# Kernel tuning notes

Measured on AMD Instinct MI355X. Metric: run time of the kernel, lower is better.

The kernel has to match this reference:

```python
import jax, jax.numpy as jnp
import numpy as np

BUCKET_SIZE = 256
LOOK_BACKWARD = 1
LOOK_FORWARD = 0  # causal


def look_around(x, backward, forward, pad_value):
    # x: (b, n_buckets, w, ...) -> (b, n_buckets, w*(backward+forward+1), ...)
    n = x.shape[1]
    pads = [(0, 0)] * x.ndim
    pads[1] = (backward, forward)
    p = jnp.pad(x, pads, constant_values=pad_value)
    return jnp.concatenate([p[:, i:i + n] for i in range(backward + forward + 1)], axis=2)


def setup_inputs() -> dict:
    key = jax.random.key(0)
    kq, kk, kv = jax.random.split(key, 3)
    shape = (2, 16, 4096, 64)  # [batch, heads, seq, head_dim]
    q = jax.random.normal(kq, shape, dtype=jnp.float32)
    k = jax.random.normal(kk, shape, dtype=jnp.float32)
    v = jax.random.normal(kv, shape, dtype=jnp.float32)
    return {"q": q, "k": k, "v": v}


def reference(q, k, v):
    shape = q.shape
    t, e = shape[-2], shape[-1]
    merge = lambda x: x.reshape(-1, t, e)
    q, k, v = merge(q), merge(k), merge(v)
    b = q.shape[0]
    buckets = t // BUCKET_SIZE

    bucket_fn = lambda x: x.reshape(b, buckets, BUCKET_SIZE, e)
    bq, bk, bv = bucket_fn(q), bucket_fn(k), bucket_fn(v)

    bk = look_around(bk, LOOK_BACKWARD, LOOK_FORWARD, 0.0)
    bv = look_around(bv, LOOK_BACKWARD, LOOK_FORWARD, 0.0)

    ticker = jnp.arange(t, dtype=jnp.int32).reshape(1, buckets, BUCKET_SIZE)
    bq_t = ticker  # (1, buckets, w)
    bq_k = look_around(ticker, LOOK_BACKWARD, LOOK_FORWARD, -1)  # (1, buckets, w*(lb+lf+1))

    dots = jnp.einsum('bnie,bnje->bnij', bq, bk) * (e ** -0.5)
    mask_value = -jnp.finfo(dots.dtype).max

    causal_mask = bq_t[:, :, :, None] < bq_k[:, :, None, :]
    pad_mask = (bq_k == -1)[:, :, None, :]
    dots = jnp.where(causal_mask | pad_mask, mask_value, dots)

    attn = jax.nn.softmax(dots, axis=-1)
    out = jnp.einsum('bnij,bnje->bnie', attn, bv)
    return out.reshape(shape)
```

## Files before the change

### kernel.cpp

```cpp
#include <hip/hip_runtime.h>

typedef __bf16 bf16x8 __attribute__((ext_vector_type(8)));
typedef float f32x4 __attribute__((ext_vector_type(4)));
typedef unsigned int u32;
typedef unsigned short u16;

#define KB 64
#define NCH 8
#define KSTR 72
#define PSP 72
#define VPS 68

static __device__ __forceinline__ u32 pack_bf2(float a, float b) {
    u16 x = __builtin_bit_cast(u16, (__bf16)a);
    u16 y = __builtin_bit_cast(u16, (__bf16)b);
    return (u32)x | ((u32)y << 16);
}

__global__ __launch_bounds__(512)
void local_attn_kernel(const float* __restrict__ qg, const float* __restrict__ kg,
                       const float* __restrict__ vg, float* __restrict__ og)
{
    __shared__ __align__(16) __bf16 sK[KB][KSTR];
    __shared__ __align__(16) u32    sVp[32][VPS];
    __shared__ __align__(16) __bf16 sP[8][2][16][PSP];

    const int bid = ((blockIdx.x & 7) << 6) | (blockIdx.x >> 3);
    const int bh = bid >> 4, bi = bid & 15;
    const int tid = threadIdx.x, w = tid >> 6;
    const int lane = tid & 63, lo = lane & 15, hi = lane >> 4;

    const long long base = (long long)bh << 18;
    const float* qb = qg + base + ((long long)bi << 14);
    const float* kb = kg + base + (((long long)(bi - 1)) << 14);
    const float* vb = vg + base + (((long long)(bi - 1)) << 14);
    float*       ob = og + base + ((long long)bi << 14);

    bf16x8 qa[2][2];
#pragma unroll
    for (int mt = 0; mt < 2; ++mt)
#pragma unroll
      for (int kk = 0; kk < 2; ++kk) {
        const float* src = qb + (w * 32 + mt * 16 + lo) * 64 + kk * 32 + 8 * hi;
        float4 f0 = *(const float4*)(src);
        float4 f1 = *(const float4*)(src + 4);
        bf16x8 t;
        t[0] = (__bf16)(f0.x * 0.125f); t[1] = (__bf16)(f0.y * 0.125f);
        t[2] = (__bf16)(f0.z * 0.125f); t[3] = (__bf16)(f0.w * 0.125f);
        t[4] = (__bf16)(f1.x * 0.125f); t[5] = (__bf16)(f1.y * 0.125f);
        t[6] = (__bf16)(f1.z * 0.125f); t[7] = (__bf16)(f1.w * 0.125f);
        qa[mt][kk] = t;
      }

    f32x4 o[2][4];
#pragma unroll
    for (int mt = 0; mt < 2; ++mt)
#pragma unroll
      for (int nt = 0; nt < 4; ++nt)
        o[mt][nt] = f32x4{0.f, 0.f, 0.f, 0.f};
    float lsum[2][4];
#pragma unroll
    for (int mt = 0; mt < 2; ++mt)
#pragma unroll
      for (int r = 0; r < 4; ++r) lsum[mt][r] = 0.0f;

    const int skey = tid >> 3;
    const int sd0  = (tid & 7) * 8;
    const int vkp  = tid >> 4;
    const int vd0  = (tid & 15) * 4;
    const float* kA = kb + (long long)skey * 64 + sd0;
    const float* vA = vb + (long long)(2 * vkp) * 64 + vd0;

    const int c0 = (bi == 0) ? 4 : 0;

    for (int c = c0; c < NCH; ++c) {
        {
            const float* p = kA + c * (KB * 64);
            float4 kf0 = *(const float4*)p;
            float4 kf1 = *(const float4*)(p + 4);
            const float* q2 = vA + c * (KB * 64);
            float4 vf0 = *(const float4*)q2;
            float4 vf1 = *(const float4*)(q2 + 64);
            bf16x8 kv;
            kv[0] = (__bf16)kf0.x; kv[1] = (__bf16)kf0.y; kv[2] = (__bf16)kf0.z; kv[3] = (__bf16)kf0.w;
            kv[4] = (__bf16)kf1.x; kv[5] = (__bf16)kf1.y; kv[6] = (__bf16)kf1.z; kv[7] = (__bf16)kf1.w;
            *(bf16x8*)&sK[skey][sd0] = kv;
            uint4 pk;
            pk.x = pack_bf2(vf0.x, vf1.x); pk.y = pack_bf2(vf0.y, vf1.y);
            pk.z = pack_bf2(vf0.z, vf1.z); pk.w = pack_bf2(vf0.w, vf1.w);
            *((uint4*)&sVp[vkp][vd0]) = pk;
        }
        __syncthreads();

        if ((c << 6) <= 32 * w + 287) {
            f32x4 s[2][4];
#pragma unroll
            for (int nt = 0; nt < 4; ++nt) {
                bf16x8 kb0 = *(const bf16x8*)&sK[nt * 16 + lo][8 * hi];
                bf16x8 kb1 = *(const bf16x8*)&sK[nt * 16 + lo][32 + 8 * hi];
                f32x4 z = f32x4{0.f, 0.f, 0.f, 0.f};
                s[0][nt] = __builtin_amdgcn_mfma_f32_16x16x32_bf16(qa[0][0], kb0, z, 0, 0, 0);
                s[0][nt] = __builtin_amdgcn_mfma_f32_16x16x32_bf16(qa[0][1], kb1, s[0][nt], 0, 0, 0);
                s[1][nt] = __builtin_amdgcn_mfma_f32_16x16x32_bf16(qa[1][0], kb0, z, 0, 0, 0);
                s[1][nt] = __builtin_amdgcn_mfma_f32_16x16x32_bf16(qa[1][1], kb1, s[1][nt], 0, 0, 0);
            }

#pragma unroll
            for (int mt = 0; mt < 2; ++mt)
#pragma unroll
              for (int nt = 0; nt < 4; ++nt) {
                const int j = (c << 6) + nt * 16 + lo;
#pragma unroll
                for (int r = 0; r < 4; ++r) {
                    const int qrow = w * 32 + mt * 16 + hi * 4 + r;
                    const float p = (j > qrow + 256) ? 0.f : __expf(s[mt][nt][r]);
                    lsum[mt][r] += p;
                    const int row = hi * 4 + r;
                    sP[w][mt][row][(nt * 16 + lo) ^ ((row & 8) << 1)] = (__bf16)p;
                }
              }

#pragma unroll
            for (int kk = 0; kk < 2; ++kk) {
                bf16x8 vbf[4];
#pragma unroll
                for (int nt = 0; nt < 4; ++nt) {
                    union { u32 d[4]; bf16x8 v; } uv;
#pragma unroll
                    for (int j = 0; j < 4; ++j)
                        uv.d[j] = sVp[kk * 16 + 4 * hi + j][nt * 16 + lo];
                    vbf[nt] = uv.v;
                }
#pragma unroll
                for (int mt = 0; mt < 2; ++mt) {
                    bf16x8 pa = *(const bf16x8*)&sP[w][mt][lo][(kk * 32 + 8 * hi) ^ ((lo & 8) << 1)];
#pragma unroll
                    for (int nt = 0; nt < 4; ++nt)
                        o[mt][nt] = __builtin_amdgcn_mfma_f32_16x16x32_bf16(pa, vbf[nt], o[mt][nt], 0, 0, 0);
                }
            }
        }
        __syncthreads();
    }

#pragma unroll
    for (int mt = 0; mt < 2; ++mt)
#pragma unroll
      for (int r = 0; r < 4; ++r) {
        float l = lsum[mt][r];
        l += __shfl_xor(l, 1, 64);
        l += __shfl_xor(l, 2, 64);
        l += __shfl_xor(l, 4, 64);
        l += __shfl_xor(l, 8, 64);
        const float inv = 1.0f / l;
        const int qrow = w * 32 + mt * 16 + hi * 4 + r;
        float* orow = ob + (long long)qrow * 64;
#pragma unroll
        for (int nt = 0; nt < 4; ++nt)
            orow[nt * 16 + lo] = o[mt][nt][r] * inv;
      }
}

extern "C" void kernel_launch(void* const* d_in, const int* in_sizes, int n_in,
                              void* d_out, int out_size, void* d_ws, size_t ws_size,
                              hipStream_t stream) {
    const float* q = (const float*)d_in[0];
    const float* k = (const float*)d_in[1];
    const float* v = (const float*)d_in[2];
    float* out = (float*)d_out;
    local_attn_kernel<<<dim3(512), dim3(512), 0, stream>>>(q, k, v, out);
}
```

Before: 40.36 us.

## Switch to 32x32 MFMA with transposed scores, register P, double-buffered K/V

Replaces the 16x16x32 MFMA layout with 32x32x16 MFMAs that compute S^T (keys x queries). The probabilities then stay in registers and are redistributed with permlane32_swap, so the shared-memory P buffer round trip is gone. K/V staging becomes double-buffered with XOR-swizzled layouts, which removes one barrier per chunk. The softmax scale is folded into Q with log2e and exp2 is used, and fully unmasked tiles skip the mask check. The cost is more complex lane mapping and a per-row shuffle in the epilogue, and the launch bounds now request higher occupancy.

```diff
diff --git a/kernel.cpp b/kernel.cpp
--- a/kernel.cpp
+++ b/kernel.cpp
@@ -1,164 +1,169 @@
 #include <hip/hip_runtime.h>
 
 typedef __bf16 bf16x8 __attribute__((ext_vector_type(8)));
-typedef float f32x4 __attribute__((ext_vector_type(4)));
+typedef float f32x16 __attribute__((ext_vector_type(16)));
+typedef int i32x2 __attribute__((ext_vector_type(2)));
 typedef unsigned int u32;
-typedef unsigned short u16;
 
-#define KB 64
 #define NCH 8
-#define KSTR 72
-#define PSP 72
-#define VPS 68
 
-static __device__ __forceinline__ u32 pack_bf2(float a, float b) {
-    u16 x = __builtin_bit_cast(u16, (__bf16)a);
-    u16 y = __builtin_bit_cast(u16, (__bf16)b);
-    return (u32)x | ((u32)y << 16);
+static __device__ __forceinline__ u32 cvt_pk_bf16(float lo, float hi) {
+    u32 r;
+    asm("v_cvt_pk_bf16_f32 %0, %1, %2" : "=v"(r) : "v"(lo), "v"(hi));
+    return r;
 }
 
-__global__ __launch_bounds__(512)
+__global__ __launch_bounds__(512, 4)
 void local_attn_kernel(const float* __restrict__ qg, const float* __restrict__ kg,
                        const float* __restrict__ vg, float* __restrict__ og)
 {
-    __shared__ __align__(16) __bf16 sK[KB][KSTR];
-    __shared__ __align__(16) u32    sVp[32][VPS];
-    __shared__ __align__(16) __bf16 sP[8][2][16][PSP];
+    __shared__ __align__(16) __bf16 sK[2][64][64];
+    __shared__ __align__(16) u32 sVp[2][64][32];
 
     const int bid = ((blockIdx.x & 7) << 6) | (blockIdx.x >> 3);
     const int bh = bid >> 4, bi = bid & 15;
     const int tid = threadIdx.x, w = tid >> 6;
-    const int lane = tid & 63, lo = lane & 15, hi = lane >> 4;
+    const int lane = tid & 63, l31 = lane & 31, h = lane >> 5;
 
     const long long base = (long long)bh << 18;
-    const float* qb = qg + base + ((long long)bi << 14);
-    const float* kb = kg + base + (((long long)(bi - 1)) << 14);
-    const float* vb = vg + base + (((long long)(bi - 1)) << 14);
-    float*       ob = og + base + ((long long)bi << 14);
+    const float* qp = qg + base + ((long long)bi << 14);
+    const float* kp = kg + base + (((long long)(bi - 1)) << 14);
+    const float* vp = vg + base + (((long long)(bi - 1)) << 14);
+    float*       op = og + base + ((long long)bi << 14);
 
-    bf16x8 qa[2][2];
+    bf16x8 qf[4];
+    {
+        const float QS = 0.18033688011112042f;
+        const float* qrow = qp + (w * 32 + l31) * 64 + 8 * h;
 #pragma unroll
-    for (int mt = 0; mt < 2; ++mt)
+        for (int ks = 0; ks < 4; ++ks) {
+            float4 f0 = *(const float4*)(qrow + ks * 16);
+            float4 f1 = *(const float4*)(qrow + ks * 16 + 4);
+            bf16x8 t;
+            t[0] = (__bf16)(f0.x * QS); t[1] = (__bf16)(f0.y * QS);
+            t[2] = (__bf16)(f0.z * QS); t[3] = (__bf16)(f0.w * QS);
+            t[4] = (__bf16)(f1.x * QS); t[5] = (__bf16)(f1.y * QS);
+            t[6] = (__bf16)(f1.z * QS); t[7] = (__bf16)(f1.w * QS);
+            qf[ks] = t;
+        }
+    }
+
+    f32x16 o0, o1;
 #pragma unroll
-      for (int kk = 0; kk < 2; ++kk) {
-        const float* src = qb + (w * 32 + mt * 16 + lo) * 64 + kk * 32 + 8 * hi;
-        float4 f0 = *(const float4*)(src);
-        float4 f1 = *(const float4*)(src + 4);
-        bf16x8 t;
-        t[0] = (__bf16)(f0.x * 0.125f); t[1] = (__bf16)(f0.y * 0.125f);
-        t[2] = (__bf16)(f0.z * 0.125f); t[3] = (__bf16)(f0.w * 0.125f);
-        t[4] = (__bf16)(f1.x * 0.125f); t[5] = (__bf16)(f1.y * 0.125f);
-        t[6] = (__bf16)(f1.z * 0.125f); t[7] = (__bf16)(f1.w * 0.125f);
-        qa[mt][kk] = t;
-      }
+    for (int i = 0; i < 16; ++i) { o0[i] = 0.f; o1[i] = 0.f; }
+    float lsum = 0.f;
 
-    f32x4 o[2][4];
-#pragma unroll
-    for (int mt = 0; mt < 2; ++mt)
-#pragma unroll
-      for (int nt = 0; nt < 4; ++nt)
-        o[mt][nt] = f32x4{0.f, 0.f, 0.f, 0.f};
-    float lsum[2][4];
-#pragma unroll
-    for (int mt = 0; mt < 2; ++mt)
-#pragma unroll
-      for (int r = 0; r < 4; ++r) lsum[mt][r] = 0.0f;
-
-    const int skey = tid >> 3;
-    const int sd0  = (tid & 7) * 8;
-    const int vkp  = tid >> 4;
-    const int vd0  = (tid & 15) * 4;
-    const float* kA = kb + (long long)skey * 64 + sd0;
-    const float* vA = vb + (long long)(2 * vkp) * 64 + vd0;
+    const int skey = tid >> 3, stg = tid & 7;
+    const int kslot = (stg ^ (skey & 7)) << 3;
+    const int vkp = tid >> 4, vd0 = (tid & 15) * 4;
+    const float* kA = kp + skey * 64 + stg * 8;
+    const float* vA = vp + (2 * vkp) * 64 + vd0;
 
     const int c0 = (bi == 0) ? 4 : 0;
+    const int qpos = w * 32 + l31;
+    const int wlim = 32 * w + 287;
+
+    int cur = 0;
+
+    auto stage = [&](int c, int buf) {
+        const float* ks_ = kA + c * (64 * 64);
+        float4 k0 = *(const float4*)ks_;
+        float4 k1 = *(const float4*)(ks_ + 4);
+        const float* vs_ = vA + c * (64 * 64);
+        float4 v0 = *(const float4*)vs_;
+        float4 v1 = *(const float4*)(vs_ + 64);
+        bf16x8 kv;
+        kv[0] = (__bf16)k0.x; kv[1] = (__bf16)k0.y; kv[2] = (__bf16)k0.z; kv[3] = (__bf16)k0.w;
+        kv[4] = (__bf16)k1.x; kv[5] = (__bf16)k1.y; kv[6] = (__bf16)k1.z; kv[7] = (__bf16)k1.w;
+        *(bf16x8*)&sK[buf][skey][kslot] = kv;
+        u32 p0 = cvt_pk_bf16(v0.x, v1.x);
+        u32 p1 = cvt_pk_bf16(v0.y, v1.y);
+        u32 p2 = cvt_pk_bf16(v0.z, v1.z);
+        u32 p3 = cvt_pk_bf16(v0.w, v1.w);
+        const int kq = vkp >> 2, kj = vkp & 3;
+        sVp[buf][vd0 + 0][((kq ^ ((vd0 + 0) & 7)) << 2) + kj] = p0;
+        sVp[buf][vd0 + 1][((kq ^ ((vd0 + 1) & 7)) << 2) + kj] = p1;
+        sVp[buf][vd0 + 2][((kq ^ ((vd0 + 2) & 7)) << 2) + kj] = p2;
+        sVp[buf][vd0 + 3][((kq ^ ((vd0 + 3) & 7)) << 2) + kj] = p3;
+    };
+
+    stage(c0, 0);
 
     for (int c = c0; c < NCH; ++c) {
-        {
-            const float* p = kA + c * (KB * 64);
-            float4 kf0 = *(const float4*)p;
-            float4 kf1 = *(const float4*)(p + 4);
-            const float* q2 = vA + c * (KB * 64);
-            float4 vf0 = *(const float4*)q2;
-            float4 vf1 = *(const float4*)(q2 + 64);
-            bf16x8 kv;
-            kv[0] = (__bf16)kf0.x; kv[1] = (__bf16)kf0.y; kv[2] = (__bf16)kf0.z; kv[3] = (__bf16)kf0.w;
-            kv[4] = (__bf16)kf1.x; kv[5] = (__bf16)kf1.y; kv[6] = (__bf16)kf1.z; kv[7] = (__bf16)kf1.w;
-            *(bf16x8*)&sK[skey][sd0] = kv;
-            uint4 pk;
-            pk.x = pack_bf2(vf0.x, vf1.x); pk.y = pack_bf2(vf0.y, vf1.y);
-            pk.z = pack_bf2(vf0.z, vf1.z); pk.w = pack_bf2(vf0.w, vf1.w);
-            *((uint4*)&sVp[vkp][vd0]) = pk;
-        }
         __syncthreads();
+        if (c + 1 < NCH) stage(c + 1, cur ^ 1);
 
-        if ((c << 6) <= 32 * w + 287) {
-            f32x4 s[2][4];
+        const int kbase = c * 64;
 #pragma unroll
-            for (int nt = 0; nt < 4; ++nt) {
-                bf16x8 kb0 = *(const bf16x8*)&sK[nt * 16 + lo][8 * hi];
-                bf16x8 kb1 = *(const bf16x8*)&sK[nt * 16 + lo][32 + 8 * hi];
-                f32x4 z = f32x4{0.f, 0.f, 0.f, 0.f};
-                s[0][nt] = __builtin_amdgcn_mfma_f32_16x16x32_bf16(qa[0][0], kb0, z, 0, 0, 0);
-                s[0][nt] = __builtin_amdgcn_mfma_f32_16x16x32_bf16(qa[0][1], kb1, s[0][nt], 0, 0, 0);
-                s[1][nt] = __builtin_amdgcn_mfma_f32_16x16x32_bf16(qa[1][0], kb0, z, 0, 0, 0);
-                s[1][nt] = __builtin_amdgcn_mfma_f32_16x16x32_bf16(qa[1][1], kb1, s[1][nt], 0, 0, 0);
+        for (int kt = 0; kt < 2; ++kt) {
+            if (kbase + 32 * kt > wlim) continue;
+
+            const int key = kt * 32 + l31;
+            const int ksw = key & 7;
+            bf16x8 kfa[4];
+#pragma unroll
+            for (int ks = 0; ks < 4; ++ks)
+                kfa[ks] = *(const bf16x8*)&sK[cur][key][((ks * 2 + h) ^ ksw) << 3];
+            f32x16 s;
+#pragma unroll
+            for (int i = 0; i < 16; ++i) s[i] = 0.f;
+#pragma unroll
+            for (int ks = 0; ks < 4; ++ks)
+                s = __builtin_amdgcn_mfma_f32_32x32x16_bf16(kfa[ks], qf[ks], s, 0, 0, 0);
+
+            float pv[16];
+            const int jb = kbase + 32 * kt + 4 * h;
+            if (kbase + 32 * kt + 31 <= 32 * w + 256) {
+#pragma unroll
+                for (int r = 0; r < 16; ++r) {
+                    pv[r] = __builtin_amdgcn_exp2f(s[r]);
+                    lsum += pv[r];
+                }
+            } else {
+#pragma unroll
+                for (int r = 0; r < 16; ++r) {
+                    const int j = jb + (r & 3) + 8 * (r >> 2);
+                    float e = __builtin_amdgcn_exp2f(s[r]);
+                    pv[r] = (j > qpos + 256) ? 0.f : e;
+                    lsum += pv[r];
+                }
             }
 
+            u32 wds[8];
 #pragma unroll
-            for (int mt = 0; mt < 2; ++mt)
-#pragma unroll
-              for (int nt = 0; nt < 4; ++nt) {
-                const int j = (c << 6) + nt * 16 + lo;
-#pragma unroll
-                for (int r = 0; r < 4; ++r) {
-                    const int qrow = w * 32 + mt * 16 + hi * 4 + r;
-                    const float p = (j > qrow + 256) ? 0.f : __expf(s[mt][nt][r]);
-                    lsum[mt][r] += p;
-                    const int row = hi * 4 + r;
-                    sP[w][mt][row][(nt * 16 + lo) ^ ((row & 8) << 1)] = (__bf16)p;
-                }
-              }
+            for (int m = 0; m < 8; ++m)
+                wds[m] = cvt_pk_bf16(pv[2 * m], pv[2 * m + 1]);
 
 #pragma unroll
-            for (int kk = 0; kk < 2; ++kk) {
-                bf16x8 vbf[4];
-#pragma unroll
-                for (int nt = 0; nt < 4; ++nt) {
-                    union { u32 d[4]; bf16x8 v; } uv;
-#pragma unroll
-                    for (int j = 0; j < 4; ++j)
-                        uv.d[j] = sVp[kk * 16 + 4 * hi + j][nt * 16 + lo];
-                    vbf[nt] = uv.v;
-                }
-#pragma unroll
-                for (int mt = 0; mt < 2; ++mt) {
-                    bf16x8 pa = *(const bf16x8*)&sP[w][mt][lo][(kk * 32 + 8 * hi) ^ ((lo & 8) << 1)];
-#pragma unroll
-                    for (int nt = 0; nt < 4; ++nt)
-                        o[mt][nt] = __builtin_amdgcn_mfma_f32_16x16x32_bf16(pa, vbf[nt], o[mt][nt], 0, 0, 0);
-                }
+            for (int kis = 0; kis < 2; ++kis) {
+                i32x2 r02 = __builtin_amdgcn_permlane32_swap(
+                    (int)wds[4 * kis + 0], (int)wds[4 * kis + 2], false, false);
+                i32x2 r13 = __builtin_amdgcn_permlane32_swap(
+                    (int)wds[4 * kis + 1], (int)wds[4 * kis + 3], false, false);
+                union { u32 u[4]; bf16x8 b; } pu;
+                pu.u[0] = (u32)r02.x; pu.u[1] = (u32)r13.x;
+                pu.u[2] = (u32)r02.y; pu.u[3] = (u32)r13.y;
+
+                const int slot = ((kt * 2 + kis) * 2 + h) ^ (l31 & 7);
+                bf16x8 vb0 = *(const bf16x8*)&sVp[cur][l31][slot << 2];
+                bf16x8 vb1 = *(const bf16x8*)&sVp[cur][32 + l31][slot << 2];
+                o0 = __builtin_amdgcn_mfma_f32_32x32x16_bf16(pu.b, vb0, o0, 0, 0, 0);
+                o1 = __builtin_amdgcn_mfma_f32_32x32x16_bf16(pu.b, vb1, o1, 0, 0, 0);
             }
         }
-        __syncthreads();
+        cur ^= 1;
     }
 
+    lsum += __shfl_xor(lsum, 32, 64);
+    const float inv = 1.0f / lsum;
 #pragma unroll
-    for (int mt = 0; mt < 2; ++mt)
-#pragma unroll
-      for (int r = 0; r < 4; ++r) {
-        float l = lsum[mt][r];
-        l += __shfl_xor(l, 1, 64);
-        l += __shfl_xor(l, 2, 64);
-        l += __shfl_xor(l, 4, 64);
-        l += __shfl_xor(l, 8, 64);
-        const float inv = 1.0f / l;
-        const int qrow = w * 32 + mt * 16 + hi * 4 + r;
-        float* orow = ob + (long long)qrow * 64;
-#pragma unroll
-        for (int nt = 0; nt < 4; ++nt)
-            orow[nt * 16 + lo] = o[mt][nt][r] * inv;
-      }
+    for (int r = 0; r < 16; ++r) {
+        const int qr = (r & 3) + 8 * (r >> 2) + 4 * h;
+        const float iq = __shfl(inv, qr, 64);
+        float* orow = op + (w * 32 + qr) * 64;
+        orow[l31]      = o0[r] * iq;
+        orow[32 + l31] = o1[r] * iq;
+    }
 }
 
 extern "C" void kernel_launch(void* const* d_in, const int* in_sizes, int n_in,
```

After: 35.91 us. 1.12x faster.
